# Kernel tuning notes

Hardware: AMD Instinct MI355X
Metric: run time of the kernel (lower is better)

The kernel has to match this reference:

```python
import jax, jax.numpy as jnp
import numpy as np

B, S, D, H = 2, 2048, 1024, 16
DEPTH = D // H


def setup_inputs() -> dict:
    key = jax.random.key(0)
    ks = jax.random.split(key, 12)
    def dense_init(kw, kb, fan_in, fan_out):
        lim = float(np.sqrt(6.0 / (fan_in + fan_out)))
        W = jax.random.uniform(kw, (fan_in, fan_out), jnp.float32, -lim, lim)
        b = jnp.zeros((fan_out,), jnp.float32)
        return W, b
    Wq, bq = dense_init(ks[0], ks[1], D, D)
    Wk, bk = dense_init(ks[2], ks[3], D, D)
    Wv, bv = dense_init(ks[4], ks[5], D, D)
    Wo, bo = dense_init(ks[6], ks[7], D, D)
    return {
        "v": jax.random.normal(ks[8], (B, S, D), jnp.float32),
        "k": jax.random.normal(ks[9], (B, S, D), jnp.float32),
        "q": jax.random.normal(ks[10], (B, S, D), jnp.float32),
        "mask": jnp.zeros((B, 1, 1, S), jnp.float32),
        "Wq": Wq, "bq": bq, "Wk": Wk, "bk": bk,
        "Wv": Wv, "bv": bv, "Wo": Wo, "bo": bo,
    }


def _split_heads(x):
    # (B, S, D) -> (B, H, S, depth)
    b, s, _ = x.shape
    return x.reshape(b, s, H, DEPTH).transpose(0, 2, 1, 3)


def reference(v, k, q, mask, Wq, bq, Wk, bk, Wv, bv, Wo, bo):
    qh = _split_heads(q @ Wq + bq)  # (B,H,S,depth)
    kh = _split_heads(k @ Wk + bk)
    vh = _split_heads(v @ Wv + bv)

    scale = 1.0 / jnp.sqrt(jnp.float32(DEPTH))
    logits = jnp.einsum('bhqd,bhkd->bhqk', qh, kh) * scale  # (B,H,S,S)

    s = logits.shape[-1]
    look_ahead = jnp.triu(jnp.ones((s, s), jnp.float32), k=1)  # 1 above diag
    m = jnp.maximum(mask, look_ahead)  # broadcast (B,1,1,S) vs (S,S)
    logits = logits + m * (-1e17)

    attn = jax.nn.softmax(logits, axis=-1)
    out = jnp.einsum('bhqk,bhkd->bhqd', attn, vh)  # (B,H,S,depth)
    out = out.transpose(0, 2, 1, 3).reshape(q.shape[0], -1, D)  # (B,S,D)
    out = out @ Wo + bo
    return out, attn
```

## Files before the change

### kernel.cpp

```cpp
#include <hip/hip_runtime.h>
#include <hip/hip_bf16.h>

#define BB 2
#define SS 2048
#define DD 1024
#define HH 16
#define DEP 64

typedef short bf16x8 __attribute__((ext_vector_type(8)));
typedef float f32x4 __attribute__((ext_vector_type(4)));
typedef unsigned short us8 __attribute__((ext_vector_type(8)));

static __device__ __forceinline__ unsigned short f2bf(float f) {
    unsigned int u = __float_as_uint(f);
    u += 0x7FFFu + ((u >> 16) & 1u);
    return (unsigned short)(u >> 16);
}

__device__ __forceinline__ void gl_lds16(const void* g, void* l) {
    __builtin_amdgcn_global_load_lds(
        (const __attribute__((address_space(1))) unsigned int*)g,
        (__attribute__((address_space(3))) unsigned int*)l, 16, 0, 0);
}

__device__ __forceinline__ void lds_fence() {
    asm volatile("s_waitcnt lgkmcnt(0)" ::: "memory");
}

__global__ __launch_bounds__(256) void conv_bf16(
    const float* __restrict__ q, const float* __restrict__ k,
    const float* __restrict__ v, unsigned short* __restrict__ qb,
    unsigned short* __restrict__ kb, unsigned short* __restrict__ vb)
{
    const int z = blockIdx.z;
    const float* src = (z == 0) ? q : (z == 1) ? k : v;
    unsigned short* dst = (z == 0) ? qb : (z == 1) ? kb : vb;
    size_t i = ((size_t)blockIdx.x * 256 + threadIdx.x) * 8;
    float4 a = *(const float4*)(src + i);
    float4 b = *(const float4*)(src + i + 4);
    us8 o;
    o[0] = f2bf(a.x); o[1] = f2bf(a.y); o[2] = f2bf(a.z); o[3] = f2bf(a.w);
    o[4] = f2bf(b.x); o[5] = f2bf(b.y); o[6] = f2bf(b.z); o[7] = f2bf(b.w);
    *(us8*)(dst + i) = o;
}

__global__ __launch_bounds__(256) void trans_w(
    const float* __restrict__ Wq, const float* __restrict__ Wk,
    const float* __restrict__ Wv, const float* __restrict__ Wo,
    unsigned short* __restrict__ Wt)
{
    __shared__ unsigned short T[64][72];
    const int z = blockIdx.z;
    const float* W = (z == 0) ? Wq : (z == 1) ? Wk : (z == 2) ? Wv : Wo;
    unsigned short* D = Wt + (size_t)z * 1024 * 1024;
    const int k0 = blockIdx.y * 64, n0 = blockIdx.x * 64;
    const int t = threadIdx.x;
    #pragma unroll
    for (int it = 0; it < 4; ++it) {
        int id = t + it * 256;
        int kk = id >> 4;
        int nn = (id & 15) * 4;
        float4 x = *(const float4*)(W + (size_t)(k0 + kk) * 1024 + n0 + nn);
        T[kk][nn + 0] = f2bf(x.x); T[kk][nn + 1] = f2bf(x.y);
        T[kk][nn + 2] = f2bf(x.z); T[kk][nn + 3] = f2bf(x.w);
    }
    __syncthreads();
    #pragma unroll
    for (int it = 0; it < 2; ++it) {
        int id = t + it * 256;
        int nn = id >> 3;
        int c8 = (id & 7) * 8;
        us8 o;
        #pragma unroll
        for (int j = 0; j < 8; ++j) o[j] = T[c8 + j][nn];
        *(us8*)(D + (size_t)(n0 + nn) * 1024 + k0 + c8) = o;
    }
}

template <int MODE>
__device__ __forceinline__ void gemm_bt_body(
    const unsigned short* __restrict__ A, const unsigned short* __restrict__ Bt,
    const float* __restrict__ bias, unsigned short* __restrict__ OutB,
    float* __restrict__ OutF)
{
    __shared__ unsigned short As[2][128 * 32];
    __shared__ unsigned short Bs[2][128 * 32];
    const int t = threadIdx.x;
    const int m0 = blockIdx.y * 128, n0 = blockIdx.x * 128;
    const int w = t >> 6, lane = t & 63, g = lane >> 4, li = lane & 15;
    const int wr = (w & 1) * 64, wc = (w >> 1) * 64;
    const int lrow = lane >> 2, lcol = (lane & 3) * 8;
    const int c0 = w * 2, c1 = w * 2 + 1;
    const int row0 = c0 * 16 + lrow, row1 = c1 * 16 + lrow;

    f32x4 acc[4][4] = {};

    auto stage = [&](int buf, int k0) {
        gl_lds16(A  + (size_t)(m0 + row0) * 1024 + k0 + lcol, &As[buf][c0 * 512]);
        gl_lds16(A  + (size_t)(m0 + row1) * 1024 + k0 + lcol, &As[buf][c1 * 512]);
        gl_lds16(Bt + (size_t)(n0 + row0) * 1024 + k0 + lcol, &Bs[buf][c0 * 512]);
        gl_lds16(Bt + (size_t)(n0 + row1) * 1024 + k0 + lcol, &Bs[buf][c1 * 512]);
    };
    auto compute = [&](int buf) {
        bf16x8 af[4], bfr[4];
        #pragma unroll
        for (int i = 0; i < 4; ++i)
            af[i] = *(const bf16x8*)&As[buf][(wr + i * 16 + li) * 32 + g * 8];
        #pragma unroll
        for (int j = 0; j < 4; ++j)
            bfr[j] = *(const bf16x8*)&Bs[buf][(wc + j * 16 + li) * 32 + g * 8];
        #pragma unroll
        for (int i = 0; i < 4; ++i)
            #pragma unroll
            for (int j = 0; j < 4; ++j)
                acc[i][j] = __builtin_amdgcn_mfma_f32_16x16x32_bf16(
                    af[i], bfr[j], acc[i][j], 0, 0, 0);
    };

    stage(0, 0);
    for (int k0 = 0; k0 < 1024 - 32; k0 += 32) {
        const int cur = (k0 >> 5) & 1;
        stage(cur ^ 1, k0 + 32);
        asm volatile("s_waitcnt vmcnt(4)" ::: "memory");
        __builtin_amdgcn_s_barrier();
        compute(cur);
        __builtin_amdgcn_s_barrier();
    }
    asm volatile("s_waitcnt vmcnt(0)" ::: "memory");
    __builtin_amdgcn_s_barrier();
    compute(1);

    #pragma unroll
    for (int i = 0; i < 4; ++i) {
        #pragma unroll
        for (int j = 0; j < 4; ++j) {
            int n = n0 + wc + j * 16 + li;
            float bv = bias[n];
            #pragma unroll
            for (int r = 0; r < 4; ++r) {
                int m = m0 + wr + i * 16 + g * 4 + r;
                float val = acc[i][j][r] + bv;
                if (MODE == 0) {
                    int b = m >> 11, s = m & 2047, h = n >> 6, dd = n & 63;
                    OutB[(((size_t)(b * HH + h)) * SS + s) * DEP + dd] = f2bf(val);
                } else {
                    OutF[(size_t)m * 1024 + n] = val;
                }
            }
        }
    }
}

__global__ __launch_bounds__(256) void gemm_qkv(
    const unsigned short* __restrict__ qb, const unsigned short* __restrict__ kb,
    const unsigned short* __restrict__ vb, const unsigned short* __restrict__ Wt,
    const float* __restrict__ bq, const float* __restrict__ bk,
    const float* __restrict__ bv,
    unsigned short* __restrict__ Qh, unsigned short* __restrict__ Kh,
    unsigned short* __restrict__ Vh)
{
    const int z = blockIdx.z;
    const unsigned short* A = (z == 0) ? qb : (z == 1) ? kb : vb;
    const unsigned short* B = Wt + (size_t)z * 1024 * 1024;
    const float* bi = (z == 0) ? bq : (z == 1) ? bk : bv;
    unsigned short* O = (z == 0) ? Qh : (z == 1) ? Kh : Vh;
    gemm_bt_body<0>(A, B, bi, O, nullptr);
}

__global__ __launch_bounds__(256) void gemm_o(
    const unsigned short* __restrict__ A, const unsigned short* __restrict__ Wt,
    const float* __restrict__ bo, float* __restrict__ Out)
{
    gemm_bt_body<1>(A, Wt + (size_t)3 * 1024 * 1024, bo, nullptr, Out);
}

__global__ __launch_bounds__(256) void transpose_v(
    const unsigned short* __restrict__ Vh, unsigned short* __restrict__ Vt)
{
    __shared__ unsigned short T[64][65];
    const int bh = blockIdx.y;
    const int s0 = blockIdx.x * 64;
    const int t = threadIdx.x;
    #pragma unroll
    for (int c = 0; c < 2; ++c) {
        int id = t + c * 256;
        int row = id >> 3, col8 = (id & 7) * 8;
        us8 v = *(const us8*)(Vh + ((size_t)bh * SS + s0 + row) * DEP + col8);
        #pragma unroll
        for (int i = 0; i < 8; ++i) T[row][col8 + i] = v[i];
    }
    __syncthreads();
    #pragma unroll
    for (int c = 0; c < 2; ++c) {
        int id = t + c * 256;
        int d = id >> 3, col8 = (id & 7) * 8;
        us8 v;
        #pragma unroll
        for (int i = 0; i < 8; ++i) v[i] = T[col8 + i][d];
        *(us8*)(Vt + ((size_t)bh * DEP + d) * SS + s0 + col8) = v;
    }
}

__global__ __launch_bounds__(256) void attn_kernel(
    const unsigned short* __restrict__ Qh, const unsigned short* __restrict__ Kh,
    const unsigned short* __restrict__ Vt, const float* __restrict__ mask,
    float* __restrict__ attn, unsigned short* __restrict__ out_h)
{
    __shared__ float Pf[4][2][16 * 36];
    const int bh = blockIdx.y;
    const int b = bh >> 4, h = bh & 15;
    const int t = threadIdx.x;
    const int w = t >> 6, lane = t & 63, g = lane >> 4, li = lane & 15;
    const int x = blockIdx.x;
    const int r0 = (w < 2) ? (x * 32 + w * 16) : (SS - 32 - x * 32 + (w - 2) * 16);
    const float scale = 0.125f;

    const unsigned short* Qb = Qh + (size_t)bh * SS * DEP;
    const unsigned short* Kb = Kh + (size_t)bh * SS * DEP;
    const unsigned short* Vb = Vt + (size_t)bh * DEP * SS;
    float* attn_b = attn + (size_t)bh * SS * SS;
    const float* mask_b = mask + (size_t)b * SS;

    bf16x8 aQ0 = *(const bf16x8*)(Qb + (size_t)(r0 + li) * DEP + g * 8);
    bf16x8 aQ1 = *(const bf16x8*)(Qb + (size_t)(r0 + li) * DEP + 32 + g * 8);

    float m_[4], l_[4];
    #pragma unroll
    for (int r = 0; r < 4; ++r) { m_[r] = -1e30f; l_[r] = 0.0f; }

    const int nch = ((r0 + 15) >> 6) + 1;
    for (int ch = 0; ch < nch; ++ch) {
        int cb = ch * 64;
        f32x4 c[4];
        #pragma unroll
        for (int tt = 0; tt < 4; ++tt) {
            const unsigned short* Kp = Kb + (size_t)(cb + tt * 16 + li) * DEP + g * 8;
            bf16x8 k0v = *(const bf16x8*)Kp;
            bf16x8 k1v = *(const bf16x8*)(Kp + 32);
            f32x4 z = {};
            z = __builtin_amdgcn_mfma_f32_16x16x32_bf16(aQ0, k0v, z, 0, 0, 0);
            z = __builtin_amdgcn_mfma_f32_16x16x32_bf16(aQ1, k1v, z, 0, 0, 0);
            c[tt] = z;
        }
        float mv[4];
        #pragma unroll
        for (int tt = 0; tt < 4; ++tt) mv[tt] = mask_b[cb + tt * 16 + li];
        #pragma unroll
        for (int r = 0; r < 4; ++r) {
            int row = r0 + g * 4 + r;
            float s[4];
            #pragma unroll
            for (int tt = 0; tt < 4; ++tt) {
                int col = cb + tt * 16 + li;
                float pen = fmaxf(mv[tt], (col > row) ? 1.0f : 0.0f);
                s[tt] = c[tt][r] * scale + pen * (-1e17f);
            }
            float cm = fmaxf(fmaxf(s[0], s[1]), fmaxf(s[2], s[3]));
            cm = fmaxf(cm, __shfl_xor(cm, 1));
            cm = fmaxf(cm, __shfl_xor(cm, 2));
            cm = fmaxf(cm, __shfl_xor(cm, 4));
            cm = fmaxf(cm, __shfl_xor(cm, 8));
            float mn = fmaxf(m_[r], cm);
            float ps = __expf(s[0] - mn) + __expf(s[1] - mn) +
                       __expf(s[2] - mn) + __expf(s[3] - mn);
            ps += __shfl_xor(ps, 1);
            ps += __shfl_xor(ps, 2);
            ps += __shfl_xor(ps, 4);
            ps += __shfl_xor(ps, 8);
            l_[r] = l_[r] * __expf(m_[r] - mn) + ps;
            m_[r] = mn;
        }
    }
    float rl[4];
    #pragma unroll
    for (int r = 0; r < 4; ++r) rl[r] = 1.0f / l_[r];

    f32x4 o[4] = {};
    const int jjc = ((r0 + 15) >> 5) + 1;

    bf16x8 kc[4], kn[4];
    {
        const unsigned short* Kp0 = Kb + (size_t)(0 + li) * DEP + g * 8;
        const unsigned short* Kp1 = Kb + (size_t)(16 + li) * DEP + g * 8;
        kc[0] = *(const bf16x8*)Kp0; kc[1] = *(const bf16x8*)(Kp0 + 32);
        kc[2] = *(const bf16x8*)Kp1; kc[3] = *(const bf16x8*)(Kp1 + 32);
    }

    for (int jj = 0; jj < jjc; ++jj) {
        int cb = jj * 32;
        float* Pw = &Pf[w][jj & 1][0];
        bf16x8 vf[4];
        #pragma unroll
        for (int tt = 0; tt < 4; ++tt)
            vf[tt] = *(const bf16x8*)(Vb + (size_t)(tt * 16 + li) * SS + cb + g * 8);
        if (jj + 1 < jjc) {
            const unsigned short* Kp0 = Kb + (size_t)(cb + 32 + li) * DEP + g * 8;
            const unsigned short* Kp1 = Kb + (size_t)(cb + 48 + li) * DEP + g * 8;
            kn[0] = *(const bf16x8*)Kp0; kn[1] = *(const bf16x8*)(Kp0 + 32);
            kn[2] = *(const bf16x8*)Kp1; kn[3] = *(const bf16x8*)(Kp1 + 32);
        }
        #pragma unroll
        for (int hh = 0; hh < 2; ++hh) {
            int ct = cb + hh * 16;
            f32x4 c = {};
            c = __builtin_amdgcn_mfma_f32_16x16x32_bf16(aQ0, kc[hh * 2 + 0], c, 0, 0, 0);
            c = __builtin_amdgcn_mfma_f32_16x16x32_bf16(aQ1, kc[hh * 2 + 1], c, 0, 0, 0);
            float mv = mask_b[ct + li];
            #pragma unroll
            for (int r = 0; r < 4; ++r) {
                int row = r0 + g * 4 + r;
                float pen = fmaxf(mv, (ct + li > row) ? 1.0f : 0.0f);
                float s = c[r] * scale + pen * (-1e17f);
                Pw[(g * 4 + r) * 36 + hh * 16 + li] = __expf(s - m_[r]) * rl[r];
            }
        }
        lds_fence();
        #pragma unroll
        for (int it = 0; it < 2; ++it) {
            int rloc = it * 8 + (lane >> 3);
            int c4 = (lane & 7) * 4;
            f32x4 val = *(const f32x4*)&Pw[rloc * 36 + c4];
            __builtin_nontemporal_store(
                val, (f32x4*)(attn_b + (size_t)(r0 + rloc) * SS + cb + c4));
        }
        float pf[8];
        *(f32x4*)&pf[0] = *(const f32x4*)&Pw[li * 36 + g * 8];
        *(f32x4*)&pf[4] = *(const f32x4*)&Pw[li * 36 + g * 8 + 4];
        bf16x8 aP;
        #pragma unroll
        for (int i = 0; i < 8; ++i) aP[i] = (short)f2bf(pf[i]);
        #pragma unroll
        for (int tt = 0; tt < 4; ++tt)
            o[tt] = __builtin_amdgcn_mfma_f32_16x16x32_bf16(aP, vf[tt], o[tt], 0, 0, 0);
        kc[0] = kn[0]; kc[1] = kn[1]; kc[2] = kn[2]; kc[3] = kn[3];
    }

    for (int cb = jjc * 32; cb < SS; cb += 64) {
        int col = cb + li * 4;
        if (col < SS) {
            f32x4 z4 = {0.f, 0.f, 0.f, 0.f};
            #pragma unroll
            for (int r = 0; r < 4; ++r) {
                int row = r0 + g * 4 + r;
                __builtin_nontemporal_store(
                    z4, (f32x4*)(attn_b + (size_t)row * SS + col));
            }
        }
    }

    unsigned short* Ow = (unsigned short*)&Pf[w][0][0];
    #pragma unroll
    for (int tt = 0; tt < 4; ++tt)
        #pragma unroll
        for (int r = 0; r < 4; ++r)
            Ow[(g * 4 + r) * 72 + tt * 16 + li] = f2bf(o[tt][r]);
    lds_fence();
    #pragma unroll
    for (int it = 0; it < 2; ++it) {
        int rloc = it * 8 + (lane >> 3);
        int c8 = (lane & 7) * 8;
        us8 val = *(const us8*)&Ow[rloc * 72 + c8];
        *(us8*)(out_h + ((size_t)b * SS + r0 + rloc) * DD + h * DEP + c8) = val;
    }
}

extern "C" void kernel_launch(void* const* d_in, const int* in_sizes, int n_in,
                              void* d_out, int out_size, void* d_ws, size_t ws_size,
                              hipStream_t stream) {
    const float* v    = (const float*)d_in[0];
    const float* k    = (const float*)d_in[1];
    const float* q    = (const float*)d_in[2];
    const float* mask = (const float*)d_in[3];
    const float* Wq   = (const float*)d_in[4];
    const float* bq   = (const float*)d_in[5];
    const float* Wk   = (const float*)d_in[6];
    const float* bk   = (const float*)d_in[7];
    const float* Wv   = (const float*)d_in[8];
    const float* bv   = (const float*)d_in[9];
    const float* Wo   = (const float*)d_in[10];
    const float* bo   = (const float*)d_in[11];

    char* ws = (char*)d_ws;
    const size_t MB = 1 << 20;
    unsigned short* qb   = (unsigned short*)(ws + 0 * MB);
    unsigned short* kb   = (unsigned short*)(ws + 8 * MB);
    unsigned short* vb   = (unsigned short*)(ws + 16 * MB);
    unsigned short* Qh   = (unsigned short*)(ws + 24 * MB);
    unsigned short* Kh   = (unsigned short*)(ws + 32 * MB);
    unsigned short* Vh   = (unsigned short*)(ws + 40 * MB);
    unsigned short* Wt   = (unsigned short*)(ws + 48 * MB);
    unsigned short* out_h = qb;
    unsigned short* Vt    = kb;

    float* out_f = (float*)d_out;
    float* attn  = out_f + (size_t)BB * SS * DD;

    conv_bf16<<<dim3(2048, 1, 3), 256, 0, stream>>>(q, k, v, qb, kb, vb);
    trans_w<<<dim3(16, 16, 4), 256, 0, stream>>>(Wq, Wk, Wv, Wo, Wt);
    gemm_qkv<<<dim3(8, 32, 3), 256, 0, stream>>>(qb, kb, vb, Wt, bq, bk, bv,
                                                 Qh, Kh, Vh);
    transpose_v<<<dim3(32, 32), 256, 0, stream>>>(Vh, Vt);
    attn_kernel<<<dim3(32, 32), 256, 0, stream>>>(Qh, Kh, Vt, mask, attn, out_h);
    gemm_o<<<dim3(8, 32), 256, 0, stream>>>(out_h, Wt, bo, out_f);
}
```

Baseline: 789.1 us.

## Fuse V transpose into QKV GEMM, defer softmax reductions, retile output GEMM

```diff
diff --git a/kernel.cpp b/kernel.cpp
--- a/kernel.cpp
+++ b/kernel.cpp
@@ -10,6 +10,7 @@
 typedef short bf16x8 __attribute__((ext_vector_type(8)));
 typedef float f32x4 __attribute__((ext_vector_type(4)));
 typedef unsigned short us8 __attribute__((ext_vector_type(8)));
+typedef unsigned short us4 __attribute__((ext_vector_type(4)));
 
 static __device__ __forceinline__ unsigned short f2bf(float f) {
     unsigned int u = __float_as_uint(f);
@@ -80,8 +81,7 @@
 template <int MODE>
 __device__ __forceinline__ void gemm_bt_body(
     const unsigned short* __restrict__ A, const unsigned short* __restrict__ Bt,
-    const float* __restrict__ bias, unsigned short* __restrict__ OutB,
-    float* __restrict__ OutF)
+    const float* __restrict__ bias, unsigned short* __restrict__ OutB)
 {
     __shared__ unsigned short As[2][128 * 32];
     __shared__ unsigned short Bs[2][128 * 32];
@@ -136,16 +136,22 @@
         for (int j = 0; j < 4; ++j) {
             int n = n0 + wc + j * 16 + li;
             float bv = bias[n];
-            #pragma unroll
-            for (int r = 0; r < 4; ++r) {
-                int m = m0 + wr + i * 16 + g * 4 + r;
-                float val = acc[i][j][r] + bv;
-                if (MODE == 0) {
+            if (MODE == 0) {
+                #pragma unroll
+                for (int r = 0; r < 4; ++r) {
+                    int m = m0 + wr + i * 16 + g * 4 + r;
+                    float val = acc[i][j][r] + bv;
                     int b = m >> 11, s = m & 2047, h = n >> 6, dd = n & 63;
                     OutB[(((size_t)(b * HH + h)) * SS + s) * DEP + dd] = f2bf(val);
-                } else {
-                    OutF[(size_t)m * 1024 + n] = val;
                 }
+            } else {
+                int mb = m0 + wr + i * 16 + g * 4;
+                int b = mb >> 11, s = mb & 2047;
+                int h = n >> 6, dd = n & 63;
+                us4 o4;
+                #pragma unroll
+                for (int r = 0; r < 4; ++r) o4[r] = f2bf(acc[i][j][r] + bv);
+                *(us4*)(OutB + ((size_t)((b * HH + h) * DEP + dd)) * SS + s) = o4;
             }
         }
     }
@@ -157,47 +163,84 @@
     const float* __restrict__ bq, const float* __restrict__ bk,
     const float* __restrict__ bv,
     unsigned short* __restrict__ Qh, unsigned short* __restrict__ Kh,
-    unsigned short* __restrict__ Vh)
+    unsigned short* __restrict__ Vt)
 {
     const int z = blockIdx.z;
     const unsigned short* A = (z == 0) ? qb : (z == 1) ? kb : vb;
     const unsigned short* B = Wt + (size_t)z * 1024 * 1024;
     const float* bi = (z == 0) ? bq : (z == 1) ? bk : bv;
-    unsigned short* O = (z == 0) ? Qh : (z == 1) ? Kh : Vh;
-    gemm_bt_body<0>(A, B, bi, O, nullptr);
+    if (z == 2) {
+        gemm_bt_body<2>(A, B, bi, Vt);
+    } else {
+        unsigned short* O = (z == 0) ? Qh : Kh;
+        gemm_bt_body<0>(A, B, bi, O);
+    }
 }
 
 __global__ __launch_bounds__(256) void gemm_o(
-    const unsigned short* __restrict__ A, const unsigned short* __restrict__ Wt,
+    const unsigned short* __restrict__ A, const unsigned short* __restrict__ Wt4,
     const float* __restrict__ bo, float* __restrict__ Out)
 {
-    gemm_bt_body<1>(A, Wt + (size_t)3 * 1024 * 1024, bo, nullptr, Out);
-}
-
-__global__ __launch_bounds__(256) void transpose_v(
-    const unsigned short* __restrict__ Vh, unsigned short* __restrict__ Vt)
-{
-    __shared__ unsigned short T[64][65];
-    const int bh = blockIdx.y;
-    const int s0 = blockIdx.x * 64;
+    const unsigned short* Bt = Wt4 + (size_t)3 * 1024 * 1024;
+    __shared__ unsigned short As[2][128 * 32];
+    __shared__ unsigned short Bs[2][64 * 32];
     const int t = threadIdx.x;
-    #pragma unroll
-    for (int c = 0; c < 2; ++c) {
-        int id = t + c * 256;
-        int row = id >> 3, col8 = (id & 7) * 8;
-        us8 v = *(const us8*)(Vh + ((size_t)bh * SS + s0 + row) * DEP + col8);
-        #pragma unroll
-        for (int i = 0; i < 8; ++i) T[row][col8 + i] = v[i];
-    }
-    __syncthreads();
-    #pragma unroll
-    for (int c = 0; c < 2; ++c) {
-        int id = t + c * 256;
-        int d = id >> 3, col8 = (id & 7) * 8;
-        us8 v;
-        #pragma unroll
-        for (int i = 0; i < 8; ++i) v[i] = T[col8 + i][d];
-        *(us8*)(Vt + ((size_t)bh * DEP + d) * SS + s0 + col8) = v;
+    const int m0 = blockIdx.y * 128, n0 = blockIdx.x * 64;
+    const int w = t >> 6, lane = t & 63, g = lane >> 4, li = lane & 15;
+    const int wr = w * 32;
+    const int lrow = lane >> 2, lcol = (lane & 3) * 8;
+    const int ca0 = w * 2, ca1 = w * 2 + 1;
+    const int rowa0 = ca0 * 16 + lrow, rowa1 = ca1 * 16 + lrow;
+    const int rowb = w * 16 + lrow;
+
+    f32x4 acc[2][4] = {};
+
+    auto stage = [&](int buf, int k0) {
+        gl_lds16(A  + (size_t)(m0 + rowa0) * 1024 + k0 + lcol, &As[buf][ca0 * 512]);
+        gl_lds16(A  + (size_t)(m0 + rowa1) * 1024 + k0 + lcol, &As[buf][ca1 * 512]);
+        gl_lds16(Bt + (size_t)(n0 + rowb) * 1024 + k0 + lcol, &Bs[buf][w * 512]);
+    };
+    auto compute = [&](int buf) {
+        bf16x8 af[2], bfr[4];
+        #pragma unroll
+        for (int i = 0; i < 2; ++i)
+            af[i] = *(const bf16x8*)&As[buf][(wr + i * 16 + li) * 32 + g * 8];
+        #pragma unroll
+        for (int j = 0; j < 4; ++j)
+            bfr[j] = *(const bf16x8*)&Bs[buf][(j * 16 + li) * 32 + g * 8];
+        #pragma unroll
+        for (int i = 0; i < 2; ++i)
+            #pragma unroll
+            for (int j = 0; j < 4; ++j)
+                acc[i][j] = __builtin_amdgcn_mfma_f32_16x16x32_bf16(
+                    af[i], bfr[j], acc[i][j], 0, 0, 0);
+    };
+
+    stage(0, 0);
+    for (int k0 = 0; k0 < 1024 - 32; k0 += 32) {
+        const int cur = (k0 >> 5) & 1;
+        stage(cur ^ 1, k0 + 32);
+        asm volatile("s_waitcnt vmcnt(3)" ::: "memory");
+        __builtin_amdgcn_s_barrier();
+        compute(cur);
+        __builtin_amdgcn_s_barrier();
+    }
+    asm volatile("s_waitcnt vmcnt(0)" ::: "memory");
+    __builtin_amdgcn_s_barrier();
+    compute(1);
+
+    #pragma unroll
+    for (int i = 0; i < 2; ++i) {
+        #pragma unroll
+        for (int j = 0; j < 4; ++j) {
+            int n = n0 + j * 16 + li;
+            float bv = bo[n];
+            #pragma unroll
+            for (int r = 0; r < 4; ++r) {
+                int m = m0 + wr + i * 16 + g * 4 + r;
+                Out[(size_t)m * 1024 + n] = acc[i][j][r] + bv;
+            }
+        }
     }
 }
 
@@ -224,9 +267,9 @@
     bf16x8 aQ0 = *(const bf16x8*)(Qb + (size_t)(r0 + li) * DEP + g * 8);
     bf16x8 aQ1 = *(const bf16x8*)(Qb + (size_t)(r0 + li) * DEP + 32 + g * 8);
 
-    float m_[4], l_[4];
-    #pragma unroll
-    for (int r = 0; r < 4; ++r) { m_[r] = -1e30f; l_[r] = 0.0f; }
+    float mL[4], lL[4];
+    #pragma unroll
+    for (int r = 0; r < 4; ++r) { mL[r] = -1e30f; lL[r] = 0.0f; }
 
     const int nch = ((r0 + 15) >> 6) + 1;
     for (int ch = 0; ch < nch; ++ch) {
@@ -256,24 +299,28 @@
                 s[tt] = c[tt][r] * scale + pen * (-1e17f);
             }
             float cm = fmaxf(fmaxf(s[0], s[1]), fmaxf(s[2], s[3]));
-            cm = fmaxf(cm, __shfl_xor(cm, 1));
-            cm = fmaxf(cm, __shfl_xor(cm, 2));
-            cm = fmaxf(cm, __shfl_xor(cm, 4));
-            cm = fmaxf(cm, __shfl_xor(cm, 8));
-            float mn = fmaxf(m_[r], cm);
-            float ps = __expf(s[0] - mn) + __expf(s[1] - mn) +
-                       __expf(s[2] - mn) + __expf(s[3] - mn);
-            ps += __shfl_xor(ps, 1);
-            ps += __shfl_xor(ps, 2);
-            ps += __shfl_xor(ps, 4);
-            ps += __shfl_xor(ps, 8);
-            l_[r] = l_[r] * __expf(m_[r] - mn) + ps;
-            m_[r] = mn;
-        }
-    }
-    float rl[4];
-    #pragma unroll
-    for (int r = 0; r < 4; ++r) rl[r] = 1.0f / l_[r];
+            float mn = fmaxf(mL[r], cm);
+            lL[r] = lL[r] * __expf(mL[r] - mn) +
+                    __expf(s[0] - mn) + __expf(s[1] - mn) +
+                    __expf(s[2] - mn) + __expf(s[3] - mn);
+            mL[r] = mn;
+        }
+    }
+    float m_[4], rl[4];
+    #pragma unroll
+    for (int r = 0; r < 4; ++r) {
+        float m = mL[r], l = lL[r];
+        #pragma unroll
+        for (int d = 1; d < 16; d <<= 1) {
+            float mo = __shfl_xor(m, d);
+            float lo = __shfl_xor(l, d);
+            float mn = fmaxf(m, mo);
+            l = l * __expf(m - mn) + lo * __expf(mo - mn);
+            m = mn;
+        }
+        m_[r] = m;
+        rl[r] = 1.0f / l;
+    }
 
     f32x4 o[4] = {};
     const int jjc = ((r0 + 15) >> 5) + 1;
@@ -387,10 +434,9 @@
     unsigned short* vb   = (unsigned short*)(ws + 16 * MB);
     unsigned short* Qh   = (unsigned short*)(ws + 24 * MB);
     unsigned short* Kh   = (unsigned short*)(ws + 32 * MB);
-    unsigned short* Vh   = (unsigned short*)(ws + 40 * MB);
+    unsigned short* Vt   = (unsigned short*)(ws + 40 * MB);
     unsigned short* Wt   = (unsigned short*)(ws + 48 * MB);
     unsigned short* out_h = qb;
-    unsigned short* Vt    = kb;
 
     float* out_f = (float*)d_out;
     float* attn  = out_f + (size_t)BB * SS * DD;
@@ -398,8 +444,7 @@
     conv_bf16<<<dim3(2048, 1, 3), 256, 0, stream>>>(q, k, v, qb, kb, vb);
     trans_w<<<dim3(16, 16, 4), 256, 0, stream>>>(Wq, Wk, Wv, Wo, Wt);
     gemm_qkv<<<dim3(8, 32, 3), 256, 0, stream>>>(qb, kb, vb, Wt, bq, bk, bv,
-                                                 Qh, Kh, Vh);
-    transpose_v<<<dim3(32, 32), 256, 0, stream>>>(Vh, Vt);
+                                                 Qh, Kh, Vt);
     attn_kernel<<<dim3(32, 32), 256, 0, stream>>>(Qh, Kh, Vt, mask, attn, out_h);
-    gemm_o<<<dim3(8, 32), 256, 0, stream>>>(out_h, Wt, bo, out_f);
-}
+    gemm_o<<<dim3(16, 32), 256, 0, stream>>>(out_h, Wt, bo, out_f);
+}
```

Result: no change. 786.7 us (-0.3%).
